# Kernel tuning notes

Hardware: AMD Instinct MI355X
Metric: run time of the kernel (lower is better)

## Reference

```python
import jax, jax.numpy as jnp
import numpy as np
import math

B, LQ, LK = 8, 1024, 1024
DQ = DK = DV = DOUT = 512
H = 8
DH = DOUT // H
EPS = 1e-5


def _ln(x, g, b):
    m = jnp.mean(x, -1, keepdims=True)
    var = jnp.mean((x - m) ** 2, -1, keepdims=True)
    return (x - m) * jax.lax.rsqrt(var + EPS) * g + b


def setup_inputs() -> dict:
    key = jax.random.key(0)
    ks = jax.random.split(key, 13)
    s = 0.02
    return {
        "q": jax.random.normal(ks[0], (B, LQ, DQ), jnp.float32),
        "k": jax.random.normal(ks[1], (B, LK, DK), jnp.float32),
        "v": jax.random.normal(ks[2], (B, LK, DV), jnp.float32),
        "mask": jax.random.randint(ks[3], (B, LK), 0, 2) > 0,  # True = masked
        "Wq": jax.random.normal(ks[4], (DOUT, DQ), jnp.float32) * s,
        "Wk": jax.random.normal(ks[5], (DOUT, DK), jnp.float32) * s,
        "Wv": jax.random.normal(ks[6], (DOUT, DV), jnp.float32) * s,
        "Wo": jax.random.normal(ks[7], (DOUT, DOUT), jnp.float32) * s,
        "bo": jnp.zeros((DOUT,), jnp.float32),
        "g1": jnp.ones((DOUT,), jnp.float32),
        "b1": jnp.zeros((DOUT,), jnp.float32),
        "g2": jnp.ones((DOUT,), jnp.float32),
        "b2": jnp.zeros((DOUT,), jnp.float32),
    }


def reference(q, k, v, mask, Wq, Wk, Wv, Wo, bo, g1, b1, g2, b2):
    qp = q @ Wq.T  # [B,Lq,D]
    kp = k @ Wk.T  # [B,Lk,D]
    vp = v @ Wv.T  # [B,Lk,D]

    # split heads: chunk(num_heads, -1) -> head h = contiguous slice of size DH
    qh = qp.reshape(B, LQ, H, DH)
    kh = kp.reshape(B, LK, H, DH)
    vh = vp.reshape(B, LK, H, DH)

    # NOTE: module divides by sqrt(dim_out), not sqrt(head_dim)
    logits = jnp.einsum("bqhd,bkhd->bhqk", qh, kh) / math.sqrt(DOUT)
    logits = jnp.where(mask[:, None, None, :], -jnp.inf, logits)
    A = jax.nn.softmax(logits, axis=-1)
    A = jnp.where(jnp.isnan(A), 0.0, A)  # masked_fill(isnan, 0)

    attn = jnp.einsum("bhqk,bkhd->bqhd", A, vh).reshape(B, LQ, DOUT)

    out = _ln(qp + attn, g1, b1)
    out = _ln(out + jax.nn.relu(out @ Wo.T + bo), g2, b2)
    return out
```

## Files before the change

kernel.cpp:

```cpp
#include <hip/hip_runtime.h>
#include <math.h>
#include <stdint.h>

#define NB 8
#define SEQ 1024
#define DMODEL 512
#define NH 8
#define HD 64
#define R_TOT (NB * SEQ)

typedef __attribute__((ext_vector_type(8))) short bf16x8;
typedef __attribute__((ext_vector_type(4))) float f32x4;

__device__ __forceinline__ short f2b(float x) {
    uint32_t u = __float_as_uint(x);
    u += 0x7FFF + ((u >> 16) & 1);
    return (short)(u >> 16);
}
__device__ __forceinline__ float b2f(short s) {
    return __uint_as_float(((uint32_t)(uint16_t)s) << 16);
}
__device__ __forceinline__ uint32_t cvtpk_bf16(float lo, float hi) {
    uint32_t r;
    asm("v_cvt_pk_bf16_f32 %0, %1, %2" : "=v"(r) : "v"(lo), "v"(hi));
    return r;
}
__device__ __forceinline__ float exp2_hw(float x) {
    float r;
    asm("v_exp_f32 %0, %1" : "=v"(r) : "v"(x));
    return r;
}
#define WAITV(N) __builtin_amdgcn_s_waitcnt(0xF70 | (N))

#define GLD_LDS16(g, l)                                                        \
    __builtin_amdgcn_global_load_lds(                                          \
        (const __attribute__((address_space(1))) uint32_t*)(g),                \
        (__attribute__((address_space(3))) uint32_t*)(l), 16, 0, 0)

__device__ __forceinline__ void xcd_swizzle(int& bx, int& by, int& bz) {
    const int gx = gridDim.x, gy = gridDim.y;
    const int nwg = gx * gy * gridDim.z;
    int id = (blockIdx.z * gy + blockIdx.y) * gx + blockIdx.x;
    int lg = (id & 7) * (nwg >> 3) + (id >> 3);
    bx = lg % gx;
    int tmp = lg / gx;
    by = tmp % gy;
    bz = tmp / gy;
}

#define N4B (R_TOT * DMODEL / 4)
#define N4W (DMODEL * DMODEL / 4)

__global__ __launch_bounds__(256)
void cvt_all(const float* __restrict__ q, const float* __restrict__ k, const float* __restrict__ v,
             const float* __restrict__ wq, const float* __restrict__ wk,
             const float* __restrict__ wv, const float* __restrict__ wo,
             short* dq, short* dk, short* dv, short* dwq, short* dwk, short* dwv, short* dwo)
{
    long i = (long)blockIdx.x * 256 + threadIdx.x;
    const float* s; short* d; long off;
    if (i < (long)N4B)          { s = q;  d = dq;  off = i; }
    else if (i < 2L * N4B)      { s = k;  d = dk;  off = i - N4B; }
    else if (i < 3L * N4B)      { s = v;  d = dv;  off = i - 2L * N4B; }
    else {
        long j = i - 3L * N4B;
        int  w = (int)(j >> 16);
        off = j & (N4W - 1);
        s = (w == 0) ? wq : (w == 1) ? wk : (w == 2) ? wv : wo;
        d = (w == 0) ? dwq : (w == 1) ? dwk : (w == 2) ? dwv : dwo;
    }
    float4 x = ((const float4*)s)[off];
    short4 o;
    o.x = f2b(x.x); o.y = f2b(x.y); o.z = f2b(x.z); o.w = f2b(x.w);
    ((short4*)d)[off] = o;
}

#define GBM 128
#define GBN 64
#define GBK 64

__device__ __forceinline__ void gemm_core(
    const short* __restrict__ A, const short* __restrict__ Bm,
    const float* __restrict__ bias, const short* __restrict__ resid,
    short* __restrict__ C,
    int N, int m0, int n0, int relu, float oscale,
    short (*As)[GBM * GBK], short (*Bs)[GBN * GBK])
{
    const int tid = threadIdx.x;
    const int l   = tid & 63, w = tid >> 6;
    const int l15 = l & 15,  l4 = l >> 4;
    const int wrow = w >> 1, wcol = w & 1;
    const int K = 512;

    f32x4 acc[4][2] = {};

    auto stageA = [&](int t, int buf) {
        #pragma unroll
        for (int j = 0; j < 4; ++j) {
            int ch  = tid + j * 256;
            int row = ch >> 3;
            int so  = (((ch & 7) * 16) ^ ((row & 7) << 4)) >> 1;
            GLD_LDS16(A + (size_t)(m0 + row) * K + t * GBK + so, &As[buf][ch * 8]);
        }
    };
    auto stageB = [&](int t, int buf) {
        #pragma unroll
        for (int j = 0; j < 2; ++j) {
            int ch  = tid + j * 256;
            int row = ch >> 3;
            int so  = (((ch & 7) * 16) ^ ((row & 7) << 4)) >> 1;
            GLD_LDS16(Bm + (size_t)(n0 + row) * K + t * GBK + so, &Bs[buf][ch * 8]);
        }
    };

    stageA(0, 0); stageB(0, 0);
    __syncthreads();

    for (int t = 0; t < 8; ++t) {
        const int cur = t & 1;
        if (t + 1 < 8) { stageA(t + 1, cur ^ 1); stageB(t + 1, cur ^ 1); }
        __builtin_amdgcn_s_setprio(1);
        #pragma unroll
        for (int kk = 0; kk < 2; ++kk) {
            bf16x8 af[4], bfr[2];
            #pragma unroll
            for (int mi = 0; mi < 4; ++mi) {
                int row = wrow * 64 + mi * 16 + l15;
                af[mi] = *(const bf16x8*)((char*)&As[cur][row * GBK] +
                                          ((kk * 64 + l4 * 16) ^ ((row & 7) << 4)));
            }
            #pragma unroll
            for (int ni = 0; ni < 2; ++ni) {
                int row = wcol * 32 + ni * 16 + l15;
                bfr[ni] = *(const bf16x8*)((char*)&Bs[cur][row * GBK] +
                                           ((kk * 64 + l4 * 16) ^ ((row & 7) << 4)));
            }
            #pragma unroll
            for (int mi = 0; mi < 4; ++mi)
                #pragma unroll
                for (int ni = 0; ni < 2; ++ni)
                    acc[mi][ni] = __builtin_amdgcn_mfma_f32_16x16x32_bf16(af[mi], bfr[ni], acc[mi][ni], 0, 0, 0);
        }
        __builtin_amdgcn_s_setprio(0);
        __syncthreads();
    }

    #pragma unroll
    for (int mi = 0; mi < 4; ++mi) {
        #pragma unroll
        for (int ni = 0; ni < 2; ++ni) {
            int col = n0 + wcol * 32 + ni * 16 + l15;
            float bb = bias ? bias[col] : 0.0f;
            #pragma unroll
            for (int r = 0; r < 4; ++r) {
                int row = m0 + wrow * 64 + mi * 16 + l4 * 4 + r;
                float vv = (acc[mi][ni][r] + bb) * oscale;
                if (relu) vv = fmaxf(vv, 0.0f);
                if (resid) vv += b2f(resid[(size_t)row * N + col]);
                C[(size_t)row * N + col] = f2b(vv);
            }
        }
    }
}

__global__ __launch_bounds__(256)
void proj3(const short* __restrict__ qb, const short* __restrict__ kb,
           const short* __restrict__ vb, const short* __restrict__ wq,
           const short* __restrict__ wv,
           short* __restrict__ qpb, short* __restrict__ vtb, float kscale)
{
    __shared__ short As[2][GBM * GBK];
    __shared__ short Bs[2][GBN * GBK];
    const size_t WSZ  = (size_t)DMODEL * DMODEL;
    const size_t SLOT = (size_t)R_TOT * DMODEL;

    int id = blockIdx.x;
    int lg = (id & 7) * 192 + (id >> 3);

    const short *A, *Bm; short* C; int N, m0, n0; float os = 1.0f;
    if (lg < 1024) {
        int bz  = lg >> 9;
        int rem = lg & 511;
        m0 = (rem >> 3) * GBM;
        n0 = (rem & 7) * GBN;
        A  = bz ? kb : qb;
        Bm = wq + bz * WSZ;
        C  = qpb + bz * SLOT;
        N  = DMODEL;
        os = bz ? kscale : 1.0f;
    } else {
        int r2  = lg - 1024;
        int b   = r2 >> 6;
        int rem = r2 & 63;
        m0 = (rem >> 4) * GBM;
        n0 = (rem & 15) * GBN;
        A  = wv;
        Bm = vb + (long)b * SEQ * DMODEL;
        C  = vtb + (long)b * DMODEL * SEQ;
        N  = SEQ;
    }
    gemm_core(A, Bm, nullptr, nullptr, C, N, m0, n0, 0, os, As, Bs);
}

__global__ __launch_bounds__(256)
void outproj(const short* __restrict__ y, const short* __restrict__ wo,
             const float* __restrict__ bias, short* __restrict__ z)
{
    __shared__ short As[2][GBM * GBK];
    __shared__ short Bs[2][GBN * GBK];
    int bx, by, bz;
    xcd_swizzle(bx, by, bz);
    gemm_core(y, wo, bias, y, z, DMODEL, by * GBM, bx * GBN, 1, 1.0f, As, Bs);
}

__global__ __launch_bounds__(512)
void attn_mfma10(const short* __restrict__ qp, const short* __restrict__ kp,
                 const short* __restrict__ vt, const int* __restrict__ mask,
                 short* __restrict__ attn)
{
    __shared__ short Kb[3][64 * 64];
    __shared__ short Vb[3][64 * 64];
    __shared__ __align__(16) char Ps[8 * 2048];
    __shared__ __align__(16) int  Mk[SEQ];

    const int tid = threadIdx.x;
    const int l   = tid & 63, w = tid >> 6;
    const int l15 = l & 15,  l4 = l >> 4;
    int qb_, h, b;
    xcd_swizzle(qb_, h, b);
    const int qrow = qb_ * 128 + w * 16 + l15;
    const size_t baseqk = ((size_t)b * SEQ) * DMODEL + h * HD;
    const size_t basev  = ((size_t)b * DMODEL + h * HD) * SEQ;

    const int ch  = tid;
    const int row = ch >> 3;
    const int so  = ((((ch & 7) * 16) ^ ((row & 7) << 4)) >> 1);
    const short* kph = kp + baseqk;
    const short* vth = vt + basev;

#define STG(t, bi) do {                                                          \
        GLD_LDS16(kph + (size_t)((t) * 64 + row) * DMODEL + so, &Kb[bi][ch * 8]); \
        GLD_LDS16(vth + (size_t)row * SEQ + (t) * 64 + so,      &Vb[bi][ch * 8]); \
    } while (0)

    const int swk   = (l15 & 7) << 4;
    const int kOff0 = l15 * 128 + ((l4 * 16) ^ swk);
    const int kOff1 = l15 * 128 + ((64 + l4 * 16) ^ swk);
    int pwOff[4];
    #pragma unroll
    for (int c = 0; c < 4; ++c)
        pwOff[c] = (l15 * 128 + c * 32 + l4 * 8) ^ swk;
    const int prOff0 = (l15 * 128 + l4 * 16) ^ swk;
    const int prOff1 = (l15 * 128 + 64 + l4 * 16) ^ swk;

    bf16x8 qf0, qf1;
    {
        const short* qr = qp + baseqk + (size_t)qrow * DMODEL + l4 * 8;
        qf0 = *(const bf16x8*)qr;
        qf1 = *(const bf16x8*)(qr + 32);
    }
    const bf16x8 ones = {0x3F80, 0x3F80, 0x3F80, 0x3F80, 0x3F80, 0x3F80, 0x3F80, 0x3F80};

    if (tid < 256) GLD_LDS16(mask + b * SEQ + tid * 4, &Mk[tid * 4]);
    STG(0, 0);
    STG(1, 1);
    __syncthreads();

    f32x4 oacc[4] = {};
    f32x4 osum = {};
    char* myPs = Ps + w * 2048;

    #pragma unroll
    for (int t = 0; t < 16; ++t) {
        const int bi = t % 3;
        if (t + 2 < 16) STG(t + 2, (t + 2) % 3);
        if (t <= 13)      WAITV(4);
        else if (t == 14) WAITV(2);
        else              WAITV(0);
        __builtin_amdgcn_s_barrier();

        f32x4 s[4];
        __builtin_amdgcn_s_setprio(1);
        #pragma unroll
        for (int c = 0; c < 4; ++c) {
            const char* kbase = (const char*)&Kb[bi][0] + c * 2048;
            bf16x8 kf0 = *(const bf16x8*)(kbase + kOff0);
            bf16x8 kf1 = *(const bf16x8*)(kbase + kOff1);
            f32x4 zz = {};
            zz = __builtin_amdgcn_mfma_f32_16x16x32_bf16(kf0, qf0, zz, 0, 0, 0);
            zz = __builtin_amdgcn_mfma_f32_16x16x32_bf16(kf1, qf1, zz, 0, 0, 0);
            s[c] = zz;
        }
        __builtin_amdgcn_s_setprio(0);

        float p[16];
        #pragma unroll
        for (int c = 0; c < 4; ++c) {
            int4 mi = *(const int4*)&Mk[t * 64 + c * 16 + l4 * 4];
            p[c * 4 + 0] = exp2_hw(mi.x ? -1.0e30f : s[c][0]);
            p[c * 4 + 1] = exp2_hw(mi.y ? -1.0e30f : s[c][1]);
            p[c * 4 + 2] = exp2_hw(mi.z ? -1.0e30f : s[c][2]);
            p[c * 4 + 3] = exp2_hw(mi.w ? -1.0e30f : s[c][3]);
        }

        #pragma unroll
        for (int c = 0; c < 4; ++c) {
            uint2 u;
            u.x = cvtpk_bf16(p[c * 4 + 0], p[c * 4 + 1]);
            u.y = cvtpk_bf16(p[c * 4 + 2], p[c * 4 + 3]);
            *(uint2*)(myPs + pwOff[c]) = u;
        }
        bf16x8 pf0 = *(const bf16x8*)(myPs + prOff0);
        bf16x8 pf1 = *(const bf16x8*)(myPs + prOff1);

        __builtin_amdgcn_s_setprio(1);
        osum = __builtin_amdgcn_mfma_f32_16x16x32_bf16(ones, pf0, osum, 0, 0, 0);
        osum = __builtin_amdgcn_mfma_f32_16x16x32_bf16(ones, pf1, osum, 0, 0, 0);
        #pragma unroll
        for (int db = 0; db < 4; ++db) {
            const char* vbase = (const char*)&Vb[bi][0] + db * 2048;
            bf16x8 vf0 = *(const bf16x8*)(vbase + kOff0);
            bf16x8 vf1 = *(const bf16x8*)(vbase + kOff1);
            oacc[db] = __builtin_amdgcn_mfma_f32_16x16x32_bf16(vf0, pf0, oacc[db], 0, 0, 0);
            oacc[db] = __builtin_amdgcn_mfma_f32_16x16x32_bf16(vf1, pf1, oacc[db], 0, 0, 0);
        }
        __builtin_amdgcn_s_setprio(0);
        __builtin_amdgcn_s_barrier();
    }
#undef STG

    float inv = (osum[0] > 0.0f) ? 1.0f / osum[0] : 0.0f;
    #pragma unroll
    for (int db = 0; db < 4; ++db) {
        const size_t eoff = baseqk + (size_t)qrow * DMODEL + db * 16 + l4 * 4;
        short4 qv = *(const short4*)(qp + eoff);
        short4 o;
        o.x = f2b(oacc[db][0] * inv + b2f(qv.x));
        o.y = f2b(oacc[db][1] * inv + b2f(qv.y));
        o.z = f2b(oacc[db][2] * inv + b2f(qv.z));
        o.w = f2b(oacc[db][3] * inv + b2f(qv.w));
        *(short4*)(attn + eoff) = o;
    }
}

__global__ __launch_bounds__(256)
void ln_one(const short* __restrict__ X, const float* __restrict__ g,
            const float* __restrict__ beta, short* __restrict__ outb,
            float* __restrict__ outf)
{
    const int row  = blockIdx.x * 4 + (threadIdx.x >> 6);
    const int lane = threadIdx.x & 63;
    const size_t off = (size_t)row * DMODEL + lane * 8;
    bf16x8 xv = *(const bf16x8*)&X[off];
    float x[8], s = 0.0f, sq = 0.0f;
    #pragma unroll
    for (int i = 0; i < 8; ++i) {
        x[i] = b2f(xv[i]);
        s += x[i];
        sq += x[i] * x[i];
    }
    #pragma unroll
    for (int o = 1; o < 64; o <<= 1) {
        s  += __shfl_xor(s,  o);
        sq += __shfl_xor(sq, o);
    }
    const float mean = s * (1.0f / DMODEL);
    const float var  = sq * (1.0f / DMODEL) - mean * mean;
    const float rs   = rsqrtf(var + 1e-5f);
    float4 g0 = *(const float4*)&g[lane * 8];
    float4 g1 = *(const float4*)&g[lane * 8 + 4];
    float4 b0 = *(const float4*)&beta[lane * 8];
    float4 b1 = *(const float4*)&beta[lane * 8 + 4];
    float gg[8] = {g0.x, g0.y, g0.z, g0.w, g1.x, g1.y, g1.z, g1.w};
    float bb[8] = {b0.x, b0.y, b0.z, b0.w, b1.x, b1.y, b1.z, b1.w};
    float y[8];
    #pragma unroll
    for (int i = 0; i < 8; ++i)
        y[i] = (x[i] - mean) * rs * gg[i] + bb[i];
    if (outb) {
        bf16x8 o;
        #pragma unroll
        for (int i = 0; i < 8; ++i) o[i] = f2b(y[i]);
        *(bf16x8*)&outb[off] = o;
    } else {
        float4 o0 = {y[0], y[1], y[2], y[3]};
        float4 o1 = {y[4], y[5], y[6], y[7]};
        *(float4*)&outf[off] = o0;
        *(float4*)&outf[off + 4] = o1;
    }
}

extern "C" void kernel_launch(void* const* d_in, const int* in_sizes, int n_in,
                              void* d_out, int out_size, void* d_ws, size_t ws_size,
                              hipStream_t stream)
{
    const float* q    = (const float*)d_in[0];
    const float* k    = (const float*)d_in[1];
    const float* v    = (const float*)d_in[2];
    const int*   mask = (const int*)  d_in[3];
    const float* Wq   = (const float*)d_in[4];
    const float* Wk   = (const float*)d_in[5];
    const float* Wv   = (const float*)d_in[6];
    const float* Wo   = (const float*)d_in[7];
    const float* bo   = (const float*)d_in[8];
    const float* g1   = (const float*)d_in[9];
    const float* b1   = (const float*)d_in[10];
    const float* g2   = (const float*)d_in[11];
    const float* bt2  = (const float*)d_in[12];
    float* out = (float*)d_out;

    short* ws = (short*)d_ws;
    const size_t WSZ  = (size_t)DMODEL * DMODEL;
    const size_t SLOT = (size_t)R_TOT * DMODEL;
    short* wq  = ws;
    short* wk  = ws + WSZ;
    short* wv  = ws + 2 * WSZ;
    short* wo  = ws + 3 * WSZ;
    short* qb  = ws + 4 * WSZ;
    short* kb  = qb + SLOT;
    short* vb  = kb + SLOT;
    short* qpb = vb + SLOT;
    short* kpb = qpb + SLOT;
    short* vtb = kpb + SLOT;
    short* at  = qb;
    short* y   = kb;
    short* z   = vb;

    const int nCvtBlocks = (3 * N4B + 4 * N4W) / 256;
    cvt_all<<<nCvtBlocks, 256, 0, stream>>>(q, k, v, Wq, Wk, Wv, Wo,
                                            qb, kb, vb, wq, wk, wv, wo);

    const float kscale = 0.06375871530f;

    proj3<<<1536, 256, 0, stream>>>(qb, kb, vb, wq, wv, qpb, vtb, kscale);

    attn_mfma10<<<dim3(SEQ / 128, NH, NB), 512, 0, stream>>>(qpb, kpb, vtb, mask, at);

    ln_one<<<R_TOT / 4, 256, 0, stream>>>(at, g1, b1, y, nullptr);

    outproj<<<dim3(DMODEL / GBN, R_TOT / GBM, 1), 256, 0, stream>>>(y, wo, bo, z);

    ln_one<<<R_TOT / 4, 256, 0, stream>>>(z, g2, bt2, nullptr, out);
}
```

Baseline: 92.82 us.

## Process two query tiles per attention block, reusing each staged K/V tile

The attention kernel now gives each workgroup 256 query rows, handled as two 128-row groups that share every K/V tile staged in LDS, so the grid shrinks to half as many blocks. The K/V pipeline moves from a three-deep buffer with explicit vmcnt waits to a two-deep buffer synchronised with __syncthreads, and the main loop is no longer force-unrolled. The aim is to halve global K/V traffic and LDS staging per query row. In exchange, only 256 blocks of 512 threads are launched, about one per CU, register pressure rises from the doubled accumulators, and loads get less prefetch lead.

```diff
diff --git a/kernel.cpp b/kernel.cpp
--- a/kernel.cpp
+++ b/kernel.cpp
@@ -30,7 +30,6 @@
     asm("v_exp_f32 %0, %1" : "=v"(r) : "v"(x));
     return r;
 }
-#define WAITV(N) __builtin_amdgcn_s_waitcnt(0xF70 | (N))
 
 #define GLD_LDS16(g, l)                                                        \
     __builtin_amdgcn_global_load_lds(                                          \
@@ -214,12 +213,12 @@
 }
 
 __global__ __launch_bounds__(512)
-void attn_mfma10(const short* __restrict__ qp, const short* __restrict__ kp,
+void attn_mfma11(const short* __restrict__ qp, const short* __restrict__ kp,
                  const short* __restrict__ vt, const int* __restrict__ mask,
                  short* __restrict__ attn)
 {
-    __shared__ short Kb[3][64 * 64];
-    __shared__ short Vb[3][64 * 64];
+    __shared__ short Kb[2][64 * 64];
+    __shared__ short Vb[2][64 * 64];
     __shared__ __align__(16) char Ps[8 * 2048];
     __shared__ __align__(16) int  Mk[SEQ];
 
@@ -228,9 +227,10 @@
     const int l15 = l & 15,  l4 = l >> 4;
     int qb_, h, b;
     xcd_swizzle(qb_, h, b);
-    const int qrow = qb_ * 128 + w * 16 + l15;
     const size_t baseqk = ((size_t)b * SEQ) * DMODEL + h * HD;
     const size_t basev  = ((size_t)b * DMODEL + h * HD) * SEQ;
+    const int qrow0 = qb_ * 256 + w * 16 + l15;
+    const int qrow1 = qrow0 + 128;
 
     const int ch  = tid;
     const int row = ch >> 3;
@@ -253,93 +253,97 @@
     const int prOff0 = (l15 * 128 + l4 * 16) ^ swk;
     const int prOff1 = (l15 * 128 + 64 + l4 * 16) ^ swk;
 
-    bf16x8 qf0, qf1;
+    bf16x8 qf[2][2];
     {
-        const short* qr = qp + baseqk + (size_t)qrow * DMODEL + l4 * 8;
-        qf0 = *(const bf16x8*)qr;
-        qf1 = *(const bf16x8*)(qr + 32);
+        const short* qr0 = qp + baseqk + (size_t)qrow0 * DMODEL + l4 * 8;
+        qf[0][0] = *(const bf16x8*)qr0;
+        qf[0][1] = *(const bf16x8*)(qr0 + 32);
+        const short* qr1 = qp + baseqk + (size_t)qrow1 * DMODEL + l4 * 8;
+        qf[1][0] = *(const bf16x8*)qr1;
+        qf[1][1] = *(const bf16x8*)(qr1 + 32);
     }
     const bf16x8 ones = {0x3F80, 0x3F80, 0x3F80, 0x3F80, 0x3F80, 0x3F80, 0x3F80, 0x3F80};
 
     if (tid < 256) GLD_LDS16(mask + b * SEQ + tid * 4, &Mk[tid * 4]);
     STG(0, 0);
-    STG(1, 1);
     __syncthreads();
 
-    f32x4 oacc[4] = {};
-    f32x4 osum = {};
+    f32x4 oacc[2][4] = {};
+    f32x4 osum[2] = {};
     char* myPs = Ps + w * 2048;
 
-    #pragma unroll
     for (int t = 0; t < 16; ++t) {
-        const int bi = t % 3;
-        if (t + 2 < 16) STG(t + 2, (t + 2) % 3);
-        if (t <= 13)      WAITV(4);
-        else if (t == 14) WAITV(2);
-        else              WAITV(0);
-        __builtin_amdgcn_s_barrier();
-
-        f32x4 s[4];
-        __builtin_amdgcn_s_setprio(1);
-        #pragma unroll
-        for (int c = 0; c < 4; ++c) {
-            const char* kbase = (const char*)&Kb[bi][0] + c * 2048;
-            bf16x8 kf0 = *(const bf16x8*)(kbase + kOff0);
-            bf16x8 kf1 = *(const bf16x8*)(kbase + kOff1);
-            f32x4 zz = {};
-            zz = __builtin_amdgcn_mfma_f32_16x16x32_bf16(kf0, qf0, zz, 0, 0, 0);
-            zz = __builtin_amdgcn_mfma_f32_16x16x32_bf16(kf1, qf1, zz, 0, 0, 0);
-            s[c] = zz;
-        }
-        __builtin_amdgcn_s_setprio(0);
-
-        float p[16];
-        #pragma unroll
-        for (int c = 0; c < 4; ++c) {
-            int4 mi = *(const int4*)&Mk[t * 64 + c * 16 + l4 * 4];
-            p[c * 4 + 0] = exp2_hw(mi.x ? -1.0e30f : s[c][0]);
-            p[c * 4 + 1] = exp2_hw(mi.y ? -1.0e30f : s[c][1]);
-            p[c * 4 + 2] = exp2_hw(mi.z ? -1.0e30f : s[c][2]);
-            p[c * 4 + 3] = exp2_hw(mi.w ? -1.0e30f : s[c][3]);
-        }
-
-        #pragma unroll
-        for (int c = 0; c < 4; ++c) {
-            uint2 u;
-            u.x = cvtpk_bf16(p[c * 4 + 0], p[c * 4 + 1]);
-            u.y = cvtpk_bf16(p[c * 4 + 2], p[c * 4 + 3]);
-            *(uint2*)(myPs + pwOff[c]) = u;
-        }
-        bf16x8 pf0 = *(const bf16x8*)(myPs + prOff0);
-        bf16x8 pf1 = *(const bf16x8*)(myPs + prOff1);
-
-        __builtin_amdgcn_s_setprio(1);
-        osum = __builtin_amdgcn_mfma_f32_16x16x32_bf16(ones, pf0, osum, 0, 0, 0);
-        osum = __builtin_amdgcn_mfma_f32_16x16x32_bf16(ones, pf1, osum, 0, 0, 0);
+        const int cur = t & 1;
+        if (t < 15) STG(t + 1, cur ^ 1);
+
+        #pragma unroll
+        for (int g = 0; g < 2; ++g) {
+            f32x4 s[4];
+            __builtin_amdgcn_s_setprio(1);
+            #pragma unroll
+            for (int c = 0; c < 4; ++c) {
+                const char* kbase = (const char*)&Kb[cur][0] + c * 2048;
+                bf16x8 kf0 = *(const bf16x8*)(kbase + kOff0);
+                bf16x8 kf1 = *(const bf16x8*)(kbase + kOff1);
+                f32x4 zz = {};
+                zz = __builtin_amdgcn_mfma_f32_16x16x32_bf16(kf0, qf[g][0], zz, 0, 0, 0);
+                zz = __builtin_amdgcn_mfma_f32_16x16x32_bf16(kf1, qf[g][1], zz, 0, 0, 0);
+                s[c] = zz;
+            }
+            __builtin_amdgcn_s_setprio(0);
+
+            float p[16];
+            #pragma unroll
+            for (int c = 0; c < 4; ++c) {
+                int4 mi = *(const int4*)&Mk[t * 64 + c * 16 + l4 * 4];
+                p[c * 4 + 0] = exp2_hw(mi.x ? -1.0e30f : s[c][0]);
+                p[c * 4 + 1] = exp2_hw(mi.y ? -1.0e30f : s[c][1]);
+                p[c * 4 + 2] = exp2_hw(mi.z ? -1.0e30f : s[c][2]);
+                p[c * 4 + 3] = exp2_hw(mi.w ? -1.0e30f : s[c][3]);
+            }
+
+            #pragma unroll
+            for (int c = 0; c < 4; ++c) {
+                uint2 u;
+                u.x = cvtpk_bf16(p[c * 4 + 0], p[c * 4 + 1]);
+                u.y = cvtpk_bf16(p[c * 4 + 2], p[c * 4 + 3]);
+                *(uint2*)(myPs + pwOff[c]) = u;
+            }
+            bf16x8 pf0 = *(const bf16x8*)(myPs + prOff0);
+            bf16x8 pf1 = *(const bf16x8*)(myPs + prOff1);
+
+            __builtin_amdgcn_s_setprio(1);
+            osum[g] = __builtin_amdgcn_mfma_f32_16x16x32_bf16(ones, pf0, osum[g], 0, 0, 0);
+            osum[g] = __builtin_amdgcn_mfma_f32_16x16x32_bf16(ones, pf1, osum[g], 0, 0, 0);
+            #pragma unroll
+            for (int db = 0; db < 4; ++db) {
+                const char* vbase = (const char*)&Vb[cur][0] + db * 2048;
+                bf16x8 vf0 = *(const bf16x8*)(vbase + kOff0);
+                bf16x8 vf1 = *(const bf16x8*)(vbase + kOff1);
+                oacc[g][db] = __builtin_amdgcn_mfma_f32_16x16x32_bf16(vf0, pf0, oacc[g][db], 0, 0, 0);
+                oacc[g][db] = __builtin_amdgcn_mfma_f32_16x16x32_bf16(vf1, pf1, oacc[g][db], 0, 0, 0);
+            }
+            __builtin_amdgcn_s_setprio(0);
+        }
+        __syncthreads();
+    }
+#undef STG
+
+    #pragma unroll
+    for (int g = 0; g < 2; ++g) {
+        const int qrow = g ? qrow1 : qrow0;
+        float inv = (osum[g][0] > 0.0f) ? 1.0f / osum[g][0] : 0.0f;
         #pragma unroll
         for (int db = 0; db < 4; ++db) {
-            const char* vbase = (const char*)&Vb[bi][0] + db * 2048;
-            bf16x8 vf0 = *(const bf16x8*)(vbase + kOff0);
-            bf16x8 vf1 = *(const bf16x8*)(vbase + kOff1);
-            oacc[db] = __builtin_amdgcn_mfma_f32_16x16x32_bf16(vf0, pf0, oacc[db], 0, 0, 0);
-            oacc[db] = __builtin_amdgcn_mfma_f32_16x16x32_bf16(vf1, pf1, oacc[db], 0, 0, 0);
-        }
-        __builtin_amdgcn_s_setprio(0);
-        __builtin_amdgcn_s_barrier();
-    }
-#undef STG
-
-    float inv = (osum[0] > 0.0f) ? 1.0f / osum[0] : 0.0f;
-    #pragma unroll
-    for (int db = 0; db < 4; ++db) {
-        const size_t eoff = baseqk + (size_t)qrow * DMODEL + db * 16 + l4 * 4;
-        short4 qv = *(const short4*)(qp + eoff);
-        short4 o;
-        o.x = f2b(oacc[db][0] * inv + b2f(qv.x));
-        o.y = f2b(oacc[db][1] * inv + b2f(qv.y));
-        o.z = f2b(oacc[db][2] * inv + b2f(qv.z));
-        o.w = f2b(oacc[db][3] * inv + b2f(qv.w));
-        *(short4*)(attn + eoff) = o;
+            const size_t eoff = baseqk + (size_t)qrow * DMODEL + db * 16 + l4 * 4;
+            short4 qv = *(const short4*)(qp + eoff);
+            short4 o;
+            o.x = f2b(oacc[g][db][0] * inv + b2f(qv.x));
+            o.y = f2b(oacc[g][db][1] * inv + b2f(qv.y));
+            o.z = f2b(oacc[g][db][2] * inv + b2f(qv.z));
+            o.w = f2b(oacc[g][db][3] * inv + b2f(qv.w));
+            *(short4*)(attn + eoff) = o;
+        }
     }
 }
 
@@ -434,7 +438,7 @@
 
     proj3<<<1536, 256, 0, stream>>>(qb, kb, vb, wq, wv, qpb, vtb, kscale);
 
-    attn_mfma10<<<dim3(SEQ / 128, NH, NB), 512, 0, stream>>>(qpb, kpb, vtb, mask, at);
+    attn_mfma11<<<dim3(SEQ / 256, NH, NB), 512, 0, stream>>>(qpb, kpb, vtb, mask, at);
 
     ln_one<<<R_TOT / 4, 256, 0, stream>>>(at, g1, b1, y, nullptr);
 
```

New measurement: 97.83 us. 1.05x slower.
